# Optimization experiments

Hardware: AMD Instinct MI355X
Metric: run time of the kernel (lower is better)

## Reference

```python
import math
import jax, jax.numpy as jnp
import numpy as np

B, S, DIM = 2, 4096, 512
HEADS, DIM_HEAD, CHUNK = 8, 64, 64
DIM_INNER = HEADS * DIM_HEAD
EPS = 1e-6


def rmsnorm(x, scale):
    var = jnp.mean(x * x, axis=-1, keepdims=True)
    return x * jax.lax.rsqrt(var + EPS) * scale


def mem_attn(p, x):
    # x: [c, dh] single chunk; tiny causal attention memory model
    q = x @ p['wq']
    k = x @ p['wk']
    v = x @ p['wv1']
    d = q.shape[-1]
    dots = (q @ k.T) * (d ** -0.5)
    c = x.shape[-2]
    mask = jnp.tril(jnp.ones((c, c), dtype=bool))
    dots = jnp.where(mask, dots, -1e9)
    attn = jax.nn.softmax(dots, axis=-1)
    hidden = attn @ v
    return jax.nn.silu(hidden) @ p['wv2']


def mem_loss(p, inp, tgt):
    pred = mem_attn(p, inp)
    return jnp.sum(jnp.mean((pred - tgt) ** 2, axis=-1))


def assoc_scan(gates, vals):
    # first-order linear recurrence y_t = g_t * y_{t-1} + v_t along axis=1
    def op(a, b):
        a1, b1 = a
        a2, b2 = b
        return a1 * a2, a2 * b1 + b2
    return jax.lax.associative_scan(op, (gates, vals), axis=1)


def setup_inputs():
    key = jax.random.key(0)
    ks = jax.random.split(key, 16)
    n = lambda k, shp, s: jax.random.normal(k, shp, dtype=jnp.float32) * s
    return {
        'seq': n(ks[0], (B, S, DIM), 1.0),
        'w_store_norm': jnp.ones((DIM,), jnp.float32),
        'w_retrieve_norm': jnp.ones((DIM,), jnp.float32),
        'w_post_norm': jnp.ones((DIM,), jnp.float32),
        'w_q': n(ks[1], (DIM, DIM_INNER), DIM ** -0.5),
        'w_kv': n(ks[2], (DIM, 2 * DIM_INNER), DIM ** -0.5),
        'w_step': n(ks[3], (DIM, HEADS), DIM ** -0.5),
        'w_mom': n(ks[4], (DIM, HEADS), DIM ** -0.5),
        'w_decay': n(ks[5], (DIM, HEADS), DIM ** -0.5),
        'w_combine': n(ks[6], (DIM_INNER, DIM), DIM_INNER ** -0.5),
        'wq': n(ks[7], (DIM_HEAD, DIM_HEAD), 0.01),
        'wk': n(ks[8], (DIM_HEAD, DIM_HEAD), 0.01),
        'wv1': n(ks[9], (DIM_HEAD, DIM_HEAD), 0.01),
        'wv2': n(ks[10], (DIM_HEAD, DIM_HEAD), 0.01),
    }


def reference(seq, w_store_norm, w_retrieve_norm, w_post_norm, w_q, w_kv,
              w_step, w_mom, w_decay, w_combine, wq, wk, wv1, wv2):
    b, s_len, d = seq.shape
    c, h, dh = CHUNK, HEADS, DIM_HEAD
    past = {'wq': wq, 'wk': wk, 'wv1': wv1, 'wv2': wv2}

    # ---------- store_memories ----------
    s = rmsnorm(seq, w_store_norm)
    n_full = (s_len // c) * c
    s = s[:, :n_full]
    nc = n_full // c

    # adaptive lr: [b,n,h] -> (b h) n -> chunk-mean [bh, nc]
    lr = jnp.exp(jax.nn.sigmoid(s @ w_step) * -15.0)
    lr = jnp.transpose(lr, (0, 2, 1)).reshape(b * h, nc, c).mean(-1)

    s_mean = s.reshape(b, nc, c, d).mean(2)  # [b, nc, d]
    mom_gate = jax.nn.sigmoid(s_mean @ w_mom)
    mom_gate = jnp.transpose(mom_gate, (0, 2, 1)).reshape(b * h, nc, 1)
    decay = jax.nn.sigmoid(s_mean @ w_decay)
    decay = jnp.transpose(decay, (0, 2, 1)).reshape(b * h, nc, 1)

    keys, values = jnp.split(s @ w_kv, 2, axis=-1)

    def chunkify(t):  # [b, n, h*dh] -> [(b h nc), c, dh]
        t = t.reshape(b, n_full, h, dh)
        t = jnp.transpose(t, (0, 2, 1, 3))
        return t.reshape(b * h * nc, c, dh)

    keys, values = chunkify(keys), chunkify(values)

    # per-chunk meta-gradients wrt shared memory-model params
    grads = jax.vmap(jax.grad(mem_loss), in_axes=(None, 0, 0))(past, keys, values)

    updates = {}
    for name in past:
        g = grads[name].reshape(b * h, nc, dh * dh)
        surprise = g * (-lr)[..., None]
        _, momentum = assoc_scan(mom_gate, surprise)
        _, upd = assoc_scan(1.0 - decay, momentum)
        updates[name] = upd.reshape(b * h, nc, dh, dh)

    wwu = {k2: past[k2][None, None] + updates[k2] for k2 in past}  # [bh, nc, dh, dh]

    # ---------- retrieve_memories ----------
    r = rmsnorm(seq, w_retrieve_norm)
    rc = r[:, c:]
    curtailed = s_len - c
    next_len = ((curtailed + 1 + c - 1) // c) * c
    pad = next_len - curtailed
    rc = jnp.pad(rc, ((0, 0), (0, pad), (0, 0)))

    q = rc @ w_q  # [b, next_len, h*dh]
    q = q.reshape(b, next_len, h, dh)
    q = jnp.transpose(q, (0, 2, 1, 3)).reshape(b * h * (next_len // c), c, dh)

    pc = {k2: v2.reshape(b * h * nc, dh, dh) for k2, v2 in wwu.items()}
    vals = jax.vmap(mem_attn)(pc, q)  # [(bh nc), c, dh]
    vals = vals.reshape(b, h, next_len, dh)
    vals = jnp.transpose(vals, (0, 2, 1, 3)).reshape(b, next_len, h * dh)
    vals = rmsnorm(vals @ w_combine, w_post_norm)
    vals = jnp.pad(vals, ((0, 0), (c, 0), (0, 0)))
    return vals[:, :-pad]
```

## Files before the change

kernel.cpp:

```cpp
#include <hip/hip_runtime.h>
#include <math.h>

constexpr int BATCH = 2, SEQ = 4096, DIM = 512, HEADS = 8, DH = 64, CH = 64;
constexpr int NC = SEQ / CH;
constexpr int BH = BATCH * HEADS;
constexpr int NCHUNK = BH * NC;
constexpr int ROWS = BATCH * SEQ;
constexpr int DI = HEADS * DH;
constexpr int TS = 64 * 72;

typedef __attribute__((ext_vector_type(8))) short short8;
typedef __attribute__((ext_vector_type(4))) short short4v;
typedef __attribute__((ext_vector_type(4))) float f32x4;

__device__ inline float sigmoidf_(float x){ return 1.f/(1.f+__expf(-x)); }
__device__ inline float dsilu_f(float x){ float s = sigmoidf_(x); return s*(1.f + x*(1.f-s)); }

__device__ inline unsigned short f2b(float f){
  union { float f; unsigned int u; } c; c.f = f;
  unsigned int u = c.u;
  unsigned int r = (u + 0x7FFFu + ((u >> 16) & 1u)) >> 16;
  return (unsigned short)r;
}
__device__ inline float b2f(unsigned short h){
  union { unsigned int u; float f; } c; c.u = ((unsigned int)h) << 16;
  return c.f;
}

struct MM { int lr, lg, rowbase, colbase; };
__device__ inline MM mmctx(){
  int tid = threadIdx.x;
  int wid = tid >> 6, lane = tid & 63;
  MM m; m.lr = lane & 15; m.lg = lane >> 4;
  m.rowbase = (wid >> 1) * 16; m.colbase = (wid & 1) * 32;
  return m;
}

template<bool SILUA>
__device__ inline void mm64(const unsigned short* A, const unsigned short* B,
                            f32x4 (&acc)[2], const MM& m)
{
  acc[0] = (f32x4){0.f,0.f,0.f,0.f};
  acc[1] = (f32x4){0.f,0.f,0.f,0.f};
  #pragma unroll
  for (int ks = 0; ks < 2; ks++){
    short8 a = *(const short8*)&A[(m.rowbase + m.lr)*72 + ks*32 + m.lg*8];
    if constexpr (SILUA){
      #pragma unroll
      for (int j = 0; j < 8; j++){
        float v = b2f((unsigned short)a[j]);
        v = v * sigmoidf_(v);
        a[j] = (short)f2b(v);
      }
    }
    #pragma unroll
    for (int ct = 0; ct < 2; ct++){
      short8 b = *(const short8*)&B[(m.colbase + ct*16 + m.lr)*72 + ks*32 + m.lg*8];
      acc[ct] = __builtin_amdgcn_mfma_f32_16x16x32_bf16(a, b, acc[ct], 0, 0, 0);
    }
  }
}

__device__ inline void storeN64(unsigned short* R, const f32x4 (&acc)[2], const MM& m, float scale){
  #pragma unroll
  for (int ct = 0; ct < 2; ct++){
    int c  = m.colbase + ct*16 + m.lr;
    int mb = m.rowbase + m.lg*4;
    #pragma unroll
    for (int r = 0; r < 4; r++) R[(mb+r)*72 + c] = f2b(acc[ct][r] * scale);
  }
}
__device__ inline void storeT64(unsigned short* T, const f32x4 (&acc)[2], const MM& m, float scale){
  #pragma unroll
  for (int ct = 0; ct < 2; ct++){
    int c  = m.colbase + ct*16 + m.lr;
    int mb = m.rowbase + m.lg*4;
    short4v p;
    #pragma unroll
    for (int r = 0; r < 4; r++) p[r] = (short)f2b(acc[ct][r] * scale);
    *(short4v*)&T[c*72 + mb] = p;
  }
}
__device__ inline void storeSC(float* S, const f32x4 (&acc)[2], const MM& m, float scale){
  #pragma unroll
  for (int ct = 0; ct < 2; ct++){
    int c  = m.colbase + ct*16 + m.lr;
    int mb = m.rowbase + m.lg*4;
    #pragma unroll
    for (int r = 0; r < 4; r++) S[(mb+r)*66 + c] = acc[ct][r] * scale;
  }
}
__device__ inline void storeGTb64(unsigned short* __restrict__ G, const f32x4 (&acc)[2],
                                  const MM& m, float scale){
  #pragma unroll
  for (int ct = 0; ct < 2; ct++){
    int c  = m.colbase + ct*16 + m.lr;
    int mb = m.rowbase + m.lg*4;
    short4v p;
    #pragma unroll
    for (int r = 0; r < 4; r++) p[r] = (short)f2b(acc[ct][r] * scale);
    *(short4v*)&G[c*64 + mb] = p;
  }
}

__device__ inline void loadTileBrow(unsigned short* R, const unsigned short* __restrict__ src,
                                    int stride, int tid){
  int i = tid >> 3, j8 = (tid & 7) * 8;
  *(short8*)&R[i*72 + j8] = *(const short8*)&src[(size_t)i*stride + j8];
}
__device__ inline void loadTileBrowT(unsigned short* R, unsigned short* T,
                                     const unsigned short* __restrict__ src,
                                     int stride, int tid){
  int i = tid >> 3, j8 = (tid & 7) * 8;
  short8 v = *(const short8*)&src[(size_t)i*stride + j8];
  *(short8*)&R[i*72 + j8] = v;
  #pragma unroll
  for (int jj = 0; jj < 8; jj++) T[(j8+jj)*72 + i] = (unsigned short)v[jj];
}

__global__ __launch_bounds__(256) void k_front(
    const float* __restrict__ seq, const float* __restrict__ wsn,
    const float* __restrict__ wrn, const float* __restrict__ wstep,
    const float* __restrict__ w_kv, const float* __restrict__ w_q,
    const float* __restrict__ wcomb,
    const float* __restrict__ wq, const float* __restrict__ wk,
    const float* __restrict__ wv1, const float* __restrict__ wv2,
    unsigned short* __restrict__ s_hi,
    unsigned short* __restrict__ rq_hi, float* __restrict__ lrp,
    unsigned short* __restrict__ wkvT_hi,
    unsigned short* __restrict__ wqT_hi, unsigned short* __restrict__ wcombT_hi,
    unsigned short* __restrict__ wpre)
{
  __shared__ float t[64][65];
  int tid = threadIdx.x;
  if (blockIdx.x >= ROWS/4){
    int blk = blockIdx.x - ROWS/4;
    if (blk < 256){
      const float* src; unsigned short *dhi;
      int R, C, bx, by;
      if (blk < 128){ src = w_kv;  dhi = wkvT_hi;  R = DIM; C = 2*DI; bx = blk & 15; by = blk >> 4; }
      else if (blk < 192){ int q = blk - 128; src = w_q;   dhi = wqT_hi;    R = DIM; C = DI;  bx = q & 7; by = q >> 3; }
      else               { int q = blk - 192; src = wcomb; dhi = wcombT_hi; R = DI;  C = DIM; bx = q & 7; by = q >> 3; }
      int c0 = bx * 64, r0 = by * 64;
      #pragma unroll
      for (int it = 0; it < 16; it++){
        int idx = it*256 + tid;
        int i = idx >> 6, j = idx & 63;
        t[i][j] = src[(size_t)(r0+i)*C + c0 + j];
      }
      __syncthreads();
      #pragma unroll
      for (int it = 0; it < 16; it++){
        int idx = it*256 + tid;
        int i = idx >> 6, j = idx & 63;
        dhi[(size_t)(c0+i)*R + r0 + j] = f2b(t[j][i]);
      }
    } else {
      int b = blk - 256;
      const float* src = (b==0) ? wq : (b==1) ? wk : (b==2) ? wv1 : wv2;
      #pragma unroll
      for (int it = 0; it < 16; it++){
        int idx = it*256 + tid;
        int i = idx >> 6, j = idx & 63;
        t[i][j] = src[i*64 + j];
      }
      __syncthreads();
      #pragma unroll
      for (int it = 0; it < 16; it++){
        int idx = it*256 + tid;
        int i = idx >> 6, j = idx & 63;
        wpre[b*4096 + i*64 + j] = f2b(t[j][i]);
        if (b == 3) wpre[4*4096 + i*64 + j] = f2b(t[i][j]);
      }
    }
    return;
  }
  int wid = tid >> 6, lane = tid & 63;
  int row = blockIdx.x * 4 + wid;
  int b = row >> 12, tt = row & 4095;
  const float* x = seq + (size_t)row * DIM;
  float4 v0 = *(const float4*)&x[lane*4];
  float4 v1 = *(const float4*)&x[256 + lane*4];
  float xv[8] = {v0.x, v0.y, v0.z, v0.w, v1.x, v1.y, v1.z, v1.w};
  float ss = 0.f;
  #pragma unroll
  for (int j = 0; j < 8; j++) ss += xv[j]*xv[j];
  #pragma unroll
  for (int m = 1; m < 64; m <<= 1) ss += __shfl_xor(ss, m);
  float rinv = rsqrtf(ss * (1.f/DIM) + 1e-6f);

  float4 w0 = *(const float4*)&wsn[lane*4];
  float4 w1 = *(const float4*)&wsn[256 + lane*4];
  float wv[8] = {w0.x, w0.y, w0.z, w0.w, w1.x, w1.y, w1.z, w1.w};
  float sv[8];
  short4v h0, h1;
  #pragma unroll
  for (int j = 0; j < 8; j++){
    sv[j] = xv[j] * rinv * wv[j];
    unsigned short hi = f2b(sv[j]);
    if (j < 4) h0[j] = (short)hi; else h1[j-4] = (short)hi;
  }
  size_t sbase = (size_t)row*DIM + lane*4;
  *(short4v*)&s_hi[sbase] = h0; *(short4v*)&s_hi[sbase + 256] = h1;

  if (tt >= CH){
    float4 r0 = *(const float4*)&wrn[lane*4];
    float4 r1 = *(const float4*)&wrn[256 + lane*4];
    float rv[8] = {r0.x, r0.y, r0.z, r0.w, r1.x, r1.y, r1.z, r1.w};
    short4v rh0, rh1;
    #pragma unroll
    for (int j = 0; j < 8; j++){
      float q = xv[j] * rinv * rv[j];
      unsigned short hi = f2b(q);
      if (j < 4) rh0[j] = (short)hi; else rh1[j-4] = (short)hi;
    }
    size_t rbase = ((size_t)b*SEQ + (tt - CH))*DIM + lane*4;
    *(short4v*)&rq_hi[rbase] = rh0; *(short4v*)&rq_hi[rbase + 256] = rh1;
  } else {
    short4v z; z[0]=0; z[1]=0; z[2]=0; z[3]=0;
    size_t rbase = ((size_t)b*SEQ + (SEQ - CH + tt))*DIM + lane*4;
    *(short4v*)&rq_hi[rbase] = z; *(short4v*)&rq_hi[rbase + 256] = z;
  }

  float acc[8] = {0.f,0.f,0.f,0.f,0.f,0.f,0.f,0.f};
  #pragma unroll
  for (int j = 0; j < 8; j++){
    int e = (j < 4) ? (lane*4 + j) : (256 + lane*4 + (j-4));
    float4 wa = *(const float4*)&wstep[e*8];
    float4 wb = *(const float4*)&wstep[e*8 + 4];
    acc[0] += sv[j]*wa.x; acc[1] += sv[j]*wa.y; acc[2] += sv[j]*wa.z; acc[3] += sv[j]*wa.w;
    acc[4] += sv[j]*wb.x; acc[5] += sv[j]*wb.y; acc[6] += sv[j]*wb.z; acc[7] += sv[j]*wb.w;
  }
  #pragma unroll
  for (int m = 1; m < 64; m <<= 1){
    #pragma unroll
    for (int h = 0; h < 8; h++) acc[h] += __shfl_xor(acc[h], m);
  }
  float a = acc[0];
  #pragma unroll
  for (int h = 1; h < 8; h++) a = (lane == h) ? acc[h] : a;
  if (lane < 8)
    lrp[(size_t)row*HEADS + lane] = __expf(-15.f * sigmoidf_(a));
}

__global__ __launch_bounds__(256, 4) void k_mid(
    const unsigned short* __restrict__ s_hi, const unsigned short* __restrict__ rq_hi,
    const unsigned short* __restrict__ wkvT_hi, const unsigned short* __restrict__ wqT_hi,
    unsigned short* __restrict__ kvb, unsigned short* __restrict__ qb,
    const float* __restrict__ lrp, const float* __restrict__ wmom,
    const float* __restrict__ wdec,
    float* __restrict__ mg, float* __restrict__ dec, float* __restrict__ lrc)
{
  __shared__ __align__(16) unsigned short AhS[128*72];
  __shared__ __align__(16) unsigned short BhS[128*72];
  int tid = threadIdx.x;
  int blk = blockIdx.x;
  if (blk >= 768){
    int bid = blk - 768;
    float* smean = (float*)AhS;
    int b = bid >> 6, ch = bid & 63;
    size_t off = ((size_t)(b*SEQ + ch*CH)) * DIM;
    for (int e = tid; e < DIM; e += 256){
      float acc = 0.f;
      for (int i = 0; i < CH; i++)
        acc += b2f(s_hi[off + (size_t)i*DIM + e]);
      smean[e] = acc * (1.f/CH);
    }
    __syncthreads();
    int gh = tid >> 5, l = tid & 31;
    float am = 0.f, ad = 0.f;
    for (int e = l; e < DIM; e += 32){
      float v = smean[e];
      am += v * wmom[e*HEADS + gh];
      ad += v * wdec[e*HEADS + gh];
    }
    const float* lrbase = lrp + ((size_t)(b*SEQ + ch*CH)) * HEADS + gh;
    float al = lrbase[(size_t)l*HEADS] + lrbase[(size_t)(l+32)*HEADS];
    #pragma unroll
    for (int m = 1; m < 32; m <<= 1){
      am += __shfl_xor(am, m);
      ad += __shfl_xor(ad, m);
      al += __shfl_xor(al, m);
    }
    if (l == 0){
      int o = (b*HEADS + gh)*NC + ch;
      mg[o]  = sigmoidf_(am);
      dec[o] = sigmoidf_(ad);
      lrc[o] = al * (1.f/CH);
    }
    return;
  }
  const unsigned short *Ahg, *Bhg; unsigned short* Cb;
  int N, nwg, bid;
  if (blk < 512){ Ahg = s_hi;  Bhg = wkvT_hi; Cb = kvb; N = 2*DI; nwg = 512; bid = blk; }
  else          { Ahg = rq_hi; Bhg = wqT_hi;  Cb = qb;  N = DI;   nwg = 256; bid = blk - 512; }
  const int K = DIM;
  int ntil = N >> 7;
  int swz = (bid & 7) * (nwg >> 3) + (bid >> 3);
  int m0 = (swz / ntil) * 128;
  int n0 = (swz % ntil) * 128;
  int wid = tid >> 6, lane = tid & 63;
  int lr = lane & 15, lg = lane >> 4;
  int wr = (wid >> 1) * 64, wc = (wid & 1) * 64;
  f32x4 acc[4][4];
  #pragma unroll
  for (int r = 0; r < 4; r++)
    #pragma unroll
    for (int c = 0; c < 4; c++) acc[r][c] = (f32x4){0.f,0.f,0.f,0.f};

  for (int k0 = 0; k0 < K; k0 += 64){
    #pragma unroll
    for (int it = 0; it < 4; it++){
      int idx = it*256 + tid;
      int row = idx >> 3, col8 = (idx & 7) * 8;
      *(short8*)&AhS[row*72 + col8] = *(const short8*)&Ahg[(size_t)(m0+row)*K + k0 + col8];
      *(short8*)&BhS[row*72 + col8] = *(const short8*)&Bhg[(size_t)(n0+row)*K + k0 + col8];
    }
    __syncthreads();
    #pragma unroll
    for (int ks = 0; ks < 2; ks++){
      short8 ah[4], bh[4];
      #pragma unroll
      for (int i = 0; i < 4; i++){
        ah[i] = *(const short8*)&AhS[(wr + i*16 + lr)*72 + ks*32 + lg*8];
        bh[i] = *(const short8*)&BhS[(wc + i*16 + lr)*72 + ks*32 + lg*8];
      }
      #pragma unroll
      for (int r = 0; r < 4; r++)
        #pragma unroll
        for (int c = 0; c < 4; c++)
          acc[r][c] = __builtin_amdgcn_mfma_f32_16x16x32_bf16(ah[r], bh[c], acc[r][c], 0, 0, 0);
    }
    __syncthreads();
  }
  #pragma unroll
  for (int rt = 0; rt < 4; rt++)
    #pragma unroll
    for (int ct = 0; ct < 4; ct++){
      int col = n0 + wc + ct*16 + lr;
      int rowb = m0 + wr + rt*16 + lg*4;
      #pragma unroll
      for (int r = 0; r < 4; r++)
        Cb[(size_t)(rowb+r)*N + col] = f2b(acc[rt][ct][r]);
    }
}

__global__ __launch_bounds__(256, 4) void k_gemm1(
    const unsigned short* __restrict__ Ahg, const unsigned short* __restrict__ Bhg,
    unsigned short* __restrict__ Cb, int M, int N, int K)
{
  __shared__ __align__(16) unsigned short AhS[128*72];
  __shared__ __align__(16) unsigned short BhS[128*72];
  int tid = threadIdx.x;
  int nwg = gridDim.x * gridDim.y;
  int bid = blockIdx.y * gridDim.x + blockIdx.x;
  int swz = (bid & 7) * (nwg >> 3) + (bid >> 3);
  int m0 = (swz / gridDim.x) * 128;
  int n0 = (swz % gridDim.x) * 128;
  int wid = tid >> 6, lane = tid & 63;
  int lr = lane & 15, lg = lane >> 4;
  int wr = (wid >> 1) * 64, wc = (wid & 1) * 64;
  f32x4 acc[4][4];
  #pragma unroll
  for (int r = 0; r < 4; r++)
    #pragma unroll
    for (int c = 0; c < 4; c++) acc[r][c] = (f32x4){0.f,0.f,0.f,0.f};

  for (int k0 = 0; k0 < K; k0 += 64){
    #pragma unroll
    for (int it = 0; it < 4; it++){
      int idx = it*256 + tid;
      int row = idx >> 3, col8 = (idx & 7) * 8;
      *(short8*)&AhS[row*72 + col8] = *(const short8*)&Ahg[(size_t)(m0+row)*K + k0 + col8];
      *(short8*)&BhS[row*72 + col8] = *(const short8*)&Bhg[(size_t)(n0+row)*K + k0 + col8];
    }
    __syncthreads();
    #pragma unroll
    for (int ks = 0; ks < 2; ks++){
      short8 ah[4], bh[4];
      #pragma unroll
      for (int i = 0; i < 4; i++){
        ah[i] = *(const short8*)&AhS[(wr + i*16 + lr)*72 + ks*32 + lg*8];
        bh[i] = *(const short8*)&BhS[(wc + i*16 + lr)*72 + ks*32 + lg*8];
      }
      #pragma unroll
      for (int r = 0; r < 4; r++)
        #pragma unroll
        for (int c = 0; c < 4; c++)
          acc[r][c] = __builtin_amdgcn_mfma_f32_16x16x32_bf16(ah[r], bh[c], acc[r][c], 0, 0, 0);
    }
    __syncthreads();
  }
  #pragma unroll
  for (int rt = 0; rt < 4; rt++)
    #pragma unroll
    for (int ct = 0; ct < 4; ct++){
      int col = n0 + wc + ct*16 + lr;
      int rowb = m0 + wr + rt*16 + lg*4;
      #pragma unroll
      for (int r = 0; r < 4; r++)
        Cb[(size_t)(rowb+r)*N + col] = f2b(acc[rt][ct][r]);
    }
}

__global__ __launch_bounds__(512) void k_grads(
    const unsigned short* __restrict__ kvb,
    const unsigned short* __restrict__ wpre,
    const float* __restrict__ lrc, unsigned short* __restrict__ g)
{
  __shared__ __align__(16) unsigned short sm[12*TS];
  __shared__ __align__(16) float SC[64*66];
  unsigned short *Xr = sm,        *XT = sm + TS,
                 *s2 = sm + 2*TS, *s3 = sm + 3*TS, *s4 = sm + 4*TS,
                 *s5 = sm + 5*TS, *s6 = sm + 6*TS, *s7 = sm + 7*TS,
                 *s8 = sm + 8*TS, *s9 = sm + 9*TS, *s10 = sm + 10*TS,
                 *s11 = sm + 11*TS;
  unsigned short *SCu = (unsigned short*)SC;
  int chunk = blockIdx.x;
  int bh = chunk >> 6, t = chunk & 63;
  int b = bh >> 3, h = bh & 7;
  int tid = threadIdx.x;
  MM M = mmctx();
  const unsigned short* xb = kvb + ((size_t)(b*SEQ + t*CH)) * (2*DI) + h*DH;
  const unsigned short* tb = xb + DI;
  float negLr = -lrc[bh*NC + t];
  f32x4 acc[2], accV[2];

  loadTileBrowT(Xr, XT, xb, 2*DI, tid);
  loadTileBrow(s2, wpre + 0*4096, 64, tid);
  loadTileBrow(s3, wpre + 1*4096, 64, tid);
  loadTileBrow(s4, wpre + 2*4096, 64, tid);
  loadTileBrow(s5, wpre + 3*4096, 64, tid);
  loadTileBrow(s6, wpre + 4*4096, 64, tid);
  __syncthreads();
  mm64<false>(Xr, s2, acc, M);
  storeN64(s7, acc, M, 1.f); storeT64(s8, acc, M, 1.f);
  mm64<false>(Xr, s3, acc, M);
  storeN64(s9, acc, M, 1.f); storeT64(s10, acc, M, 1.f);
  mm64<false>(Xr, s4, accV, M);
  storeN64(s11, accV, M, 1.f);
  __syncthreads();
  storeT64(s2, accV, M, 1.f);
  mm64<false>(s7, s9, acc, M);
  storeSC(SC, acc, M, 0.125f);
  __syncthreads();
  {
    int row = tid >> 3, q = tid & 7;
    float p[8];
    float mx = -1e30f;
    #pragma unroll
    for (int cc = 0; cc < 8; cc++){
      int col = q*8 + cc;
      float x = SC[row*66 + col];
      p[cc] = (col <= row) ? x : -1e9f;
      mx = fmaxf(mx, p[cc]);
    }
    mx = fmaxf(mx, __shfl_xor(mx, 1));
    mx = fmaxf(mx, __shfl_xor(mx, 2));
    mx = fmaxf(mx, __shfl_xor(mx, 4));
    float sum = 0.f;
    #pragma unroll
    for (int cc = 0; cc < 8; cc++){ p[cc] = __expf(p[cc] - mx); sum += p[cc]; }
    sum += __shfl_xor(sum, 1);
    sum += __shfl_xor(sum, 2);
    sum += __shfl_xor(sum, 4);
    float inv = 1.f / sum;
    #pragma unroll
    for (int cc = 0; cc < 8; cc++){
      int col = q*8 + cc;
      unsigned short hh = f2b(p[cc] * inv);
      s7[row*72 + col] = hh;
      s9[col*72 + row] = hh;
    }
  }
  __syncthreads();
  mm64<false>(s7, s2, acc, M);
  storeN64(s3, acc, M, 1.f); storeT64(s4, acc, M, 1.f);
  __syncthreads();
  mm64<true>(s3, s5, acc, M);
  #pragma unroll
  for (int ct = 0; ct < 2; ct++){
    int c  = M.colbase + ct*16 + M.lr;
    int mb = M.rowbase + M.lg*4;
    #pragma unroll
    for (int r = 0; r < 4; r++){
      float t2 = (acc[ct][r] - b2f(tb[(size_t)(mb+r)*(2*DI) + c])) * (2.f/64.f);
      unsigned short hh = f2b(t2);
      Xr[(mb+r)*72 + c] = hh;
      s2[c*72 + (mb+r)] = hh;
    }
  }
  __syncthreads();
  mm64<true>(s4, s2, acc, M);
  storeGTb64(g + ((size_t)(3*NCHUNK + chunk))*4096, acc, M, negLr);
  mm64<false>(Xr, s6, acc, M);
  #pragma unroll
  for (int ct = 0; ct < 2; ct++){
    int c  = M.colbase + ct*16 + M.lr;
    int mb = M.rowbase + M.lg*4;
    #pragma unroll
    for (int r = 0; r < 4; r++){
      float x = b2f(s3[(mb+r)*72 + c]);
      float d = acc[ct][r] * dsilu_f(x);
      unsigned short hh = f2b(d);
      s5[(mb+r)*72 + c] = hh;
      SCu[c*72 + (mb+r)] = hh;
    }
  }
  __syncthreads();
  mm64<false>(s5, s11, acc, M);
  storeN64(Xr, acc, M, 1.f);
  mm64<false>(s9, SCu, acc, M);
  storeT64(s2, acc, M, 1.f);
  __syncthreads();
  {
    int row = tid >> 3, q = tid & 7;
    float da[8], a[8], rs = 0.f;
    #pragma unroll
    for (int cc = 0; cc < 8; cc++){
      int col = q*8 + cc;
      da[cc] = b2f(Xr[row*72 + col]);
      a[cc]  = b2f(s7[row*72 + col]);
      rs += da[cc]*a[cc];
    }
    rs += __shfl_xor(rs, 1);
    rs += __shfl_xor(rs, 2);
    rs += __shfl_xor(rs, 4);
    #pragma unroll
    for (int cc = 0; cc < 8; cc++){
      int col = q*8 + cc;
      unsigned short hh = f2b(a[cc] * (da[cc] - rs));
      s3[row*72 + col] = hh;
      s6[col*72 + row] = hh;
    }
  }
  mm64<false>(XT, s2, acc, M);
  storeGTb64(g + ((size_t)(2*NCHUNK + chunk))*4096, acc, M, negLr);
  __syncthreads();
  mm64<false>(s3, s10, acc, M);
  storeT64(Xr, acc, M, 0.125f);
  mm64<false>(s6, s8, acc, M);
  storeT64(s2, acc, M, 0.125f);
  __syncthreads();
  mm64<false>(XT, Xr, acc, M);
  storeGTb64(g + ((size_t)(0*NCHUNK + chunk))*4096, acc, M, negLr);
  mm64<false>(XT, s2, acc, M);
  storeGTb64(g + ((size_t)(1*NCHUNK + chunk))*4096, acc, M, negLr);
}

__global__ __launch_bounds__(256) void k_scan(
    unsigned short* __restrict__ g, const float* __restrict__ mg, const float* __restrict__ dec,
    const float* __restrict__ wq, const float* __restrict__ wk,
    const float* __restrict__ wv1, const float* __restrict__ wv2)
{
  int idx = blockIdx.x * 256 + threadIdx.x;
  int e = (idx & 2047) * 2;
  int bh = (idx >> 11) & 15;
  int name = idx >> 15;
  const float* past = (name == 0) ? wq : (name == 1) ? wk : (name == 2) ? wv1 : wv2;
  float base0 = past[(e & 63)*64 + (e >> 6)];
  float base1 = past[((e+1) & 63)*64 + ((e+1) >> 6)];
  const float* mgb = mg + bh*NC;
  const float* dcb = dec + bh*NC;
  size_t baseoff = ((size_t)name*NCHUNK + (size_t)bh*NC)*4096 + e;
  float m0 = 0.f, u0 = 0.f, m1 = 0.f, u1 = 0.f;
  for (int t = 0; t < NC; t++){
    size_t off = baseoff + (size_t)t*4096;
    unsigned int v = *(const unsigned int*)&g[off];
    float su0 = b2f((unsigned short)(v & 0xffff));
    float su1 = b2f((unsigned short)(v >> 16));
    float gm = mgb[t], dc = dcb[t];
    m0 = gm*m0 + su0;  u0 = (1.f - dc)*u0 + m0;
    m1 = gm*m1 + su1;  u1 = (1.f - dc)*u1 + m1;
    unsigned int w = (unsigned int)f2b(base0 + u0) | ((unsigned int)f2b(base1 + u1) << 16);
    *(unsigned int*)&g[off] = w;
  }
}

__global__ __launch_bounds__(512, 4) void k_retrieve(
    const unsigned short* __restrict__ qb, const unsigned short* __restrict__ Wg,
    unsigned short* __restrict__ vals_hi)
{
  __shared__ __align__(16) unsigned short sm[6*TS];
  __shared__ __align__(16) float SC[64*66];
  unsigned short *Xr = sm,       *Wt = sm + TS,   *Qr = sm + 2*TS,
                 *Kr = sm + 3*TS, *Vt = sm + 4*TS, *Hr = sm + 5*TS;
  unsigned short *Ar = (unsigned short*)SC;
  int chunk = blockIdx.x;
  int bh = chunk >> 6, t = chunk & 63;
  int b = bh >> 3, h = bh & 7;
  int tid = threadIdx.x;
  MM M = mmctx();
  const unsigned short* xb = qb + ((size_t)(b*SEQ + t*CH)) * DI + h*DH;
  f32x4 acc[2], accV[2];

  loadTileBrow(Xr, xb, DI, tid);
  loadTileBrow(Wt, Wg + ((size_t)(0*NCHUNK + chunk))*4096, 64, tid);
  __syncthreads();
  mm64<false>(Xr, Wt, acc, M); storeN64(Qr, acc, M, 1.f);
  loadTileBrow(Hr, Wg + ((size_t)(1*NCHUNK + chunk))*4096, 64, tid);
  __syncthreads();
  mm64<false>(Xr, Hr, acc, M); storeN64(Kr, acc, M, 1.f);
  loadTileBrow(Wt, Wg + ((size_t)(2*NCHUNK + chunk))*4096, 64, tid);
  __syncthreads();
  mm64<false>(Xr, Wt, accV, M); storeT64(Vt, accV, M, 1.f);
  mm64<false>(Qr, Kr, acc, M); storeSC(SC, acc, M, 0.125f);
  loadTileBrow(Hr, Wg + ((size_t)(3*NCHUNK + chunk))*4096, 64, tid);
  __syncthreads();
  {
    int row = tid >> 3, q = tid & 7;
    float p[8];
    float mx = -1e30f;
    #pragma unroll
    for (int cc = 0; cc < 8; cc++){
      int col = q*8 + cc;
      float x = SC[row*66 + col];
      p[cc] = (col <= row) ? x : -1e9f;
      mx = fmaxf(mx, p[cc]);
    }
    mx = fmaxf(mx, __shfl_xor(mx, 1));
    mx = fmaxf(mx, __shfl_xor(mx, 2));
    mx = fmaxf(mx, __shfl_xor(mx, 4));
    float sum = 0.f;
    #pragma unroll
    for (int cc = 0; cc < 8; cc++){ p[cc] = __expf(p[cc] - mx); sum += p[cc]; }
    sum += __shfl_xor(sum, 1);
    sum += __shfl_xor(sum, 2);
    sum += __shfl_xor(sum, 4);
    float inv = 1.f / sum;
    __syncthreads();
    #pragma unroll
    for (int cc = 0; cc < 8; cc++){
      int col = q*8 + cc;
      Ar[row*72 + col] = f2b(p[cc] * inv);
    }
  }
  __syncthreads();
  mm64<false>(Ar, Vt, acc, M); storeN64(Kr, acc, M, 1.f);
  __syncthreads();
  mm64<true>(Kr, Hr, acc, M);
  #pragma unroll
  for (int ct = 0; ct < 2; ct++){
    int c  = M.colbase + ct*16 + M.lr;
    int mb = M.rowbase + M.lg*4;
    #pragma unroll
    for (int r = 0; r < 4; r++){
      size_t o = ((size_t)(b*SEQ + t*CH + mb + r))*DI + h*DH + c;
      vals_hi[o] = f2b(acc[ct][r]);
    }
  }
}

__global__ __launch_bounds__(256) void k_outnorm(
    const unsigned short* __restrict__ tmp, const float* __restrict__ wpn,
    float* __restrict__ out)
{
  int wid = threadIdx.x >> 6, lane = threadIdx.x & 63;
  int row = blockIdx.x * 4 + wid;
  int b = row >> 12, r = row & 4095;
  float* dst = out + ((size_t)b*SEQ + r) * DIM;
  if (r < CH){
    float4 z = make_float4(0.f, 0.f, 0.f, 0.f);
    *(float4*)&dst[lane*8] = z;
    *(float4*)&dst[lane*8 + 4] = z;
    return;
  }
  const unsigned short* src = tmp + ((size_t)b*SEQ + (r - CH)) * DIM;
  short8 t0 = *(const short8*)&src[lane*8];
  float xv[8];
  #pragma unroll
  for (int j = 0; j < 8; j++) xv[j] = b2f((unsigned short)t0[j]);
  float ss = 0.f;
  #pragma unroll
  for (int j = 0; j < 8; j++) ss += xv[j]*xv[j];
  #pragma unroll
  for (int m = 1; m < 64; m <<= 1) ss += __shfl_xor(ss, m);
  float rinv = rsqrtf(ss * (1.f/DIM) + 1e-6f);
  float4 o0, o1;
  o0.x = xv[0]*rinv*wpn[lane*8+0]; o0.y = xv[1]*rinv*wpn[lane*8+1];
  o0.z = xv[2]*rinv*wpn[lane*8+2]; o0.w = xv[3]*rinv*wpn[lane*8+3];
  o1.x = xv[4]*rinv*wpn[lane*8+4]; o1.y = xv[5]*rinv*wpn[lane*8+5];
  o1.z = xv[6]*rinv*wpn[lane*8+6]; o1.w = xv[7]*rinv*wpn[lane*8+7];
  *(float4*)&dst[lane*8] = o0;
  *(float4*)&dst[lane*8 + 4] = o1;
}

extern "C" void kernel_launch(void* const* d_in, const int* in_sizes, int n_in,
                              void* d_out, int out_size, void* d_ws, size_t ws_size,
                              hipStream_t stream)
{
  (void)in_sizes; (void)n_in; (void)ws_size; (void)out_size;
  const float* seq   = (const float*)d_in[0];
  const float* wsn   = (const float*)d_in[1];
  const float* wrn   = (const float*)d_in[2];
  const float* wpn   = (const float*)d_in[3];
  const float* w_q   = (const float*)d_in[4];
  const float* w_kv  = (const float*)d_in[5];
  const float* wstep = (const float*)d_in[6];
  const float* wmom  = (const float*)d_in[7];
  const float* wdec  = (const float*)d_in[8];
  const float* wcomb = (const float*)d_in[9];
  const float* wq    = (const float*)d_in[10];
  const float* wk    = (const float*)d_in[11];
  const float* wv1   = (const float*)d_in[12];
  const float* wv2   = (const float*)d_in[13];
  float* out = (float*)d_out;

  char* p = (char*)d_ws;
  unsigned short* s_hi  = (unsigned short*)p; p += (size_t)ROWS*DIM*2;
  unsigned short* rq_hi = (unsigned short*)p; p += (size_t)ROWS*DIM*2;
  unsigned short* kvb   = (unsigned short*)p; p += (size_t)ROWS*2*DI*2;
  unsigned short* qb    = (unsigned short*)p; p += (size_t)ROWS*DI*2;
  unsigned short* g     = (unsigned short*)p; p += (size_t)4*NCHUNK*4096*2;
  float* lrp            = (float*)p;          p += (size_t)ROWS*HEADS*4;
  float* mg             = (float*)p;          p += (size_t)BH*NC*4;
  float* dec            = (float*)p;          p += (size_t)BH*NC*4;
  float* lrc            = (float*)p;          p += (size_t)BH*NC*4;
  unsigned short* wkvT_hi   = (unsigned short*)p; p += (size_t)(2*DI)*DIM*2;
  unsigned short* wqT_hi    = (unsigned short*)p; p += (size_t)DI*DIM*2;
  unsigned short* wcombT_hi = (unsigned short*)p; p += (size_t)DIM*DI*2;
  unsigned short* wpre      = (unsigned short*)p; p += (size_t)5*4096*2;
  unsigned short* vals_hi   = (unsigned short*)p; p += (size_t)ROWS*DI*2;
  unsigned short* tmp = s_hi;

  k_front<<<ROWS/4 + 260, 256, 0, stream>>>(
      seq, wsn, wrn, wstep, w_kv, w_q, wcomb, wq, wk, wv1, wv2,
      s_hi, rq_hi, lrp, wkvT_hi, wqT_hi, wcombT_hi, wpre);
  k_mid<<<896, 256, 0, stream>>>(
      s_hi, rq_hi, wkvT_hi, wqT_hi, kvb, qb,
      lrp, wmom, wdec, mg, dec, lrc);
  k_grads<<<NCHUNK, 512, 0, stream>>>(kvb, wpre, lrc, g);
  k_scan<<<(4*BH*2048)/256, 256, 0, stream>>>(g, mg, dec, wq, wk, wv1, wv2);
  k_retrieve<<<NCHUNK, 512, 0, stream>>>(qb, g, vals_hi);
  k_gemm1<<<dim3(DIM/128, ROWS/128), 256, 0, stream>>>(
      vals_hi, wcombT_hi, tmp, ROWS, DIM, DI);
  k_outnorm<<<ROWS/4, 256, 0, stream>>>(tmp, wpn, out);
}
```

Baseline: 152.2 us.

## Use LDS-only barriers, prefetch scan gradients, merge retrieve tile loads

Replaces __syncthreads in the store-gradient and retrieve kernels with a barrier that waits only on LDS operations (lgkmcnt), so outstanding global stores of gradient tiles no longer stall each barrier. The scan kernel software-pipelines its strided global loads two chunks ahead, to hide load latency in the serial recurrence. The retrieve kernel loads the Q and K weight tiles together and drops one barrier, and reassigns shared buffers so the V transpose goes into the freed Wt tile. This relies on every cross-thread LDS dependency being covered by lgkmcnt(0); if any tile load writes LDS directly from global memory, a vmcnt wait would be missing.

```diff
diff --git a/kernel.cpp b/kernel.cpp
--- a/kernel.cpp
+++ b/kernel.cpp
@@ -12,6 +12,9 @@
 typedef __attribute__((ext_vector_type(8))) short short8;
 typedef __attribute__((ext_vector_type(4))) short short4v;
 typedef __attribute__((ext_vector_type(4))) float f32x4;
+
+#define LBAR() do { asm volatile("s_waitcnt lgkmcnt(0)" ::: "memory"); \
+                    __builtin_amdgcn_s_barrier(); } while (0)
 
 __device__ inline float sigmoidf_(float x){ return 1.f/(1.f+__expf(-x)); }
 __device__ inline float dsilu_f(float x){ float s = sigmoidf_(x); return s*(1.f + x*(1.f-s)); }
@@ -432,18 +435,18 @@
   loadTileBrow(s4, wpre + 2*4096, 64, tid);
   loadTileBrow(s5, wpre + 3*4096, 64, tid);
   loadTileBrow(s6, wpre + 4*4096, 64, tid);
-  __syncthreads();
+  LBAR();
   mm64<false>(Xr, s2, acc, M);
   storeN64(s7, acc, M, 1.f); storeT64(s8, acc, M, 1.f);
   mm64<false>(Xr, s3, acc, M);
   storeN64(s9, acc, M, 1.f); storeT64(s10, acc, M, 1.f);
   mm64<false>(Xr, s4, accV, M);
   storeN64(s11, accV, M, 1.f);
-  __syncthreads();
+  LBAR();
   storeT64(s2, accV, M, 1.f);
   mm64<false>(s7, s9, acc, M);
   storeSC(SC, acc, M, 0.125f);
-  __syncthreads();
+  LBAR();
   {
     int row = tid >> 3, q = tid & 7;
     float p[8];
@@ -473,10 +476,10 @@
       s9[col*72 + row] = hh;
     }
   }
-  __syncthreads();
+  LBAR();
   mm64<false>(s7, s2, acc, M);
   storeN64(s3, acc, M, 1.f); storeT64(s4, acc, M, 1.f);
-  __syncthreads();
+  LBAR();
   mm64<true>(s3, s5, acc, M);
   #pragma unroll
   for (int ct = 0; ct < 2; ct++){
@@ -490,7 +493,7 @@
       s2[c*72 + (mb+r)] = hh;
     }
   }
-  __syncthreads();
+  LBAR();
   mm64<true>(s4, s2, acc, M);
   storeGTb64(g + ((size_t)(3*NCHUNK + chunk))*4096, acc, M, negLr);
   mm64<false>(Xr, s6, acc, M);
@@ -507,12 +510,12 @@
       SCu[c*72 + (mb+r)] = hh;
     }
   }
-  __syncthreads();
+  LBAR();
   mm64<false>(s5, s11, acc, M);
   storeN64(Xr, acc, M, 1.f);
   mm64<false>(s9, SCu, acc, M);
   storeT64(s2, acc, M, 1.f);
-  __syncthreads();
+  LBAR();
   {
     int row = tid >> 3, q = tid & 7;
     float da[8], a[8], rs = 0.f;
@@ -536,12 +539,12 @@
   }
   mm64<false>(XT, s2, acc, M);
   storeGTb64(g + ((size_t)(2*NCHUNK + chunk))*4096, acc, M, negLr);
-  __syncthreads();
+  LBAR();
   mm64<false>(s3, s10, acc, M);
   storeT64(Xr, acc, M, 0.125f);
   mm64<false>(s6, s8, acc, M);
   storeT64(s2, acc, M, 0.125f);
-  __syncthreads();
+  LBAR();
   mm64<false>(XT, Xr, acc, M);
   storeGTb64(g + ((size_t)(0*NCHUNK + chunk))*4096, acc, M, negLr);
   mm64<false>(XT, s2, acc, M);
@@ -562,18 +565,21 @@
   float base1 = past[((e+1) & 63)*64 + ((e+1) >> 6)];
   const float* mgb = mg + bh*NC;
   const float* dcb = dec + bh*NC;
-  size_t baseoff = ((size_t)name*NCHUNK + (size_t)bh*NC)*4096 + e;
+  size_t off = ((size_t)name*NCHUNK + (size_t)bh*NC)*4096 + e;
   float m0 = 0.f, u0 = 0.f, m1 = 0.f, u1 = 0.f;
+  unsigned int v0 = *(const unsigned int*)&g[off];
+  unsigned int v1 = *(const unsigned int*)&g[off + 4096];
   for (int t = 0; t < NC; t++){
-    size_t off = baseoff + (size_t)t*4096;
-    unsigned int v = *(const unsigned int*)&g[off];
-    float su0 = b2f((unsigned short)(v & 0xffff));
-    float su1 = b2f((unsigned short)(v >> 16));
+    unsigned int vn = 0;
+    if (t + 2 < NC) vn = *(const unsigned int*)&g[off + 2*4096];
+    float su0 = b2f((unsigned short)(v0 & 0xffff));
+    float su1 = b2f((unsigned short)(v0 >> 16));
     float gm = mgb[t], dc = dcb[t];
     m0 = gm*m0 + su0;  u0 = (1.f - dc)*u0 + m0;
     m1 = gm*m1 + su1;  u1 = (1.f - dc)*u1 + m1;
     unsigned int w = (unsigned int)f2b(base0 + u0) | ((unsigned int)f2b(base1 + u1) << 16);
     *(unsigned int*)&g[off] = w;
+    v0 = v1; v1 = vn; off += 4096;
   }
 }
 
@@ -592,21 +598,20 @@
   int tid = threadIdx.x;
   MM M = mmctx();
   const unsigned short* xb = qb + ((size_t)(b*SEQ + t*CH)) * DI + h*DH;
-  f32x4 acc[2], accV[2];
+  f32x4 acc[2], acc2[2];
 
   loadTileBrow(Xr, xb, DI, tid);
   loadTileBrow(Wt, Wg + ((size_t)(0*NCHUNK + chunk))*4096, 64, tid);
-  __syncthreads();
-  mm64<false>(Xr, Wt, acc, M); storeN64(Qr, acc, M, 1.f);
   loadTileBrow(Hr, Wg + ((size_t)(1*NCHUNK + chunk))*4096, 64, tid);
-  __syncthreads();
-  mm64<false>(Xr, Hr, acc, M); storeN64(Kr, acc, M, 1.f);
-  loadTileBrow(Wt, Wg + ((size_t)(2*NCHUNK + chunk))*4096, 64, tid);
-  __syncthreads();
-  mm64<false>(Xr, Wt, accV, M); storeT64(Vt, accV, M, 1.f);
-  mm64<false>(Qr, Kr, acc, M); storeSC(SC, acc, M, 0.125f);
+  LBAR();
+  mm64<false>(Xr, Wt, acc, M);  storeN64(Qr, acc, M, 1.f);
+  mm64<false>(Xr, Hr, acc2, M); storeN64(Kr, acc2, M, 1.f);
+  loadTileBrow(Vt, Wg + ((size_t)(2*NCHUNK + chunk))*4096, 64, tid);
+  LBAR();
+  mm64<false>(Xr, Vt, acc, M);  storeT64(Wt, acc, M, 1.f);
+  mm64<false>(Qr, Kr, acc2, M); storeSC(SC, acc2, M, 0.125f);
   loadTileBrow(Hr, Wg + ((size_t)(3*NCHUNK + chunk))*4096, 64, tid);
-  __syncthreads();
+  LBAR();
   {
     int row = tid >> 3, q = tid & 7;
     float p[8];
@@ -628,16 +633,16 @@
     sum += __shfl_xor(sum, 2);
     sum += __shfl_xor(sum, 4);
     float inv = 1.f / sum;
-    __syncthreads();
+    LBAR();
     #pragma unroll
     for (int cc = 0; cc < 8; cc++){
       int col = q*8 + cc;
       Ar[row*72 + col] = f2b(p[cc] * inv);
     }
   }
-  __syncthreads();
-  mm64<false>(Ar, Vt, acc, M); storeN64(Kr, acc, M, 1.f);
-  __syncthreads();
+  LBAR();
+  mm64<false>(Ar, Wt, acc, M); storeN64(Kr, acc, M, 1.f);
+  LBAR();
   mm64<true>(Kr, Hr, acc, M);
   #pragma unroll
   for (int ct = 0; ct < 2; ct++){
```

Result: slower. 165.0 us (+8.4%).
